# Performance work log

Measured on AMD Instinct MI355X. Metric: run time of the kernel, lower is better.

Reference implementation:

```python
import jax, jax.numpy as jnp
import numpy as np

N, T, D, H, Da = 128, 256, 1024, 1024, 14


def setup_inputs() -> dict:
    key = jax.random.key(0)
    ks = jax.random.split(key, 6)
    x = jax.random.normal(ks[0], (N, T, D), dtype=jnp.float32)
    A = jax.random.normal(ks[1], (N, H, Da, Da), dtype=jnp.float32)
    Wx = jax.random.normal(ks[2], (D, 4 * H), dtype=jnp.float32) / np.sqrt(D)
    Wh = jax.random.normal(ks[3], (H, 4 * H), dtype=jnp.float32) / np.sqrt(H)
    Wattn = jax.random.normal(ks[4], (H, 4 * H), dtype=jnp.float32) / np.sqrt(H)
    b = jnp.zeros((4 * H,), dtype=jnp.float32)
    return {"x": x, "A": A, "Wx": Wx, "Wh": Wh, "Wattn": Wattn, "b": b}


def reference(x, A, Wx, Wh, Wattn, b):
    n, t, d = x.shape
    h_dim = A.shape[1]
    da = A.shape[2]
    scale = 1.0 / np.sqrt(h_dim).astype(np.float32)
    A_flat = A.reshape(n, h_dim, da * da)            # (N, H, P)
    h0 = jnp.mean(A_flat, axis=-1)                   # global avg pool == mean over (2,3)
    c0 = h0

    def step(carry, xt):
        h, c = carry
        # scaled dot-product attention over spatial positions
        scores = jnp.einsum('nh,nhp->np', h, A_flat) * scale   # (N, P)
        w = jax.nn.softmax(scores, axis=-1)
        attn = jnp.einsum('nhp,np->nh', A_flat, w)             # (N, H)
        # fused LSTM gates
        a = xt @ Wx + h @ Wh + attn @ Wattn + b                # (N, 4H)
        ai, af, ao, ag = jnp.split(a, 4, axis=1)
        i = jax.nn.sigmoid(ai)
        f = jax.nn.sigmoid(af)
        o = jax.nn.sigmoid(ao)
        g = jnp.tanh(ag)
        c_next = f * c + i * g
        h_next = o * jnp.tanh(c_next)
        return (h_next, c_next), h_next

    xs = jnp.swapaxes(x, 0, 1)                       # (T, N, D)
    _, hs = jax.lax.scan(step, (h0, c0), xs)         # hs: (T, N, H)
    return jnp.swapaxes(hs, 0, 1)                    # (N, T, H)
```

## Files before the change

kernel.cpp:

```cpp
#include <hip/hip_runtime.h>
#include <math.h>

typedef _Float16 f16;
typedef f16 f16x4 __attribute__((ext_vector_type(4)));
typedef f16 f16x8 __attribute__((ext_vector_type(8)));
typedef float f32x4 __attribute__((ext_vector_type(4)));

#define NB 128
#define TT 256
#define DD 1024
#define HH 1024
#define PP 196
#define K3 3072
#define FOURH 4096
#define NBLK 256
#define NTHR 512
#define WROW 3078
#define LDS_BYTES (16 * WROW * 2 + 9216 * 4)
#define BAR_U32 (8192 + 128 * 64)

__global__ void k_h0(const float* __restrict__ A, float* __restrict__ c0,
                     f16* __restrict__ act_h0) {
  int idx = blockIdx.x * 256 + threadIdx.x;
  const float4* ap = (const float4*)(A + (size_t)idx * PP);
  float s = 0.f;
#pragma unroll
  for (int i = 0; i < PP / 4; ++i) { float4 v = ap[i]; s += v.x + v.y + v.z + v.w; }
  float m = s * (1.0f / PP);
  c0[idx] = m;
  act_h0[idx] = (f16)m;
}

__global__ void k_At(const float* __restrict__ A, f16* __restrict__ A2) {
  __shared__ float tile[32][33];
  int p0 = blockIdx.x * 32, h0 = blockIdx.y * 32, n = blockIdx.z;
  for (int i = threadIdx.x; i < 1024; i += 256) {
    int r = i >> 5, c = i & 31;
    int p = p0 + c;
    float v = 0.f;
    if (p < PP) v = A[((size_t)n * HH + h0 + r) * PP + p];
    tile[r][c] = v;
  }
  __syncthreads();
  for (int i = threadIdx.x; i < 1024; i += 256) {
    int r = i >> 5, c = i & 31;
    int p = p0 + r;
    if (p < PP) A2[((size_t)n * PP + p) * HH + h0 + c] = (f16)tile[c][r];
  }
}

__global__ void k_Wt(const float* __restrict__ Wx, const float* __restrict__ Wh,
                     const float* __restrict__ Wa, f16* __restrict__ Wt) {
  __shared__ float tile[32][33];
  int k0 = blockIdx.x * 32, j0 = blockIdx.y * 32;
  const float* src; int kb;
  if (k0 < 1024)      { src = Wx; kb = k0; }
  else if (k0 < 2048) { src = Wh; kb = k0 - 1024; }
  else                { src = Wa; kb = k0 - 2048; }
  for (int i = threadIdx.x; i < 1024; i += 256) {
    int r = i >> 5, c = i & 31;
    tile[r][c] = src[(size_t)(kb + r) * FOURH + j0 + c];
  }
  __syncthreads();
  for (int i = threadIdx.x; i < 1024; i += 256) {
    int r = i >> 5, c = i & 31;
    Wt[(size_t)(j0 + r) * K3 + k0 + c] = (f16)tile[c][r];
  }
}

__global__ void k_xcvt(const float* __restrict__ x, f16* __restrict__ xh) {
  size_t i = (size_t)blockIdx.x * 256 + threadIdx.x;
  float4 v = ((const float4*)x)[i];
  f16x4 o; o[0] = (f16)v.x; o[1] = (f16)v.y; o[2] = (f16)v.z; o[3] = (f16)v.w;
  *(f16x4*)(xh + i * 4) = o;
}

__device__ __forceinline__ void bar_arrive(unsigned* base, int bx) {
  asm volatile("s_waitcnt vmcnt(0)" ::: "memory");
  unsigned lv = __hip_atomic_fetch_add(base + (bx & 15) * 64, 1u,
                                       __ATOMIC_RELAXED, __HIP_MEMORY_SCOPE_AGENT);
  if ((lv & 15u) == 15u) {
    unsigned rv = __hip_atomic_fetch_add(base + 1024, 1u,
                                         __ATOMIC_RELAXED, __HIP_MEMORY_SCOPE_AGENT);
    if ((rv & 15u) == 15u) {
      unsigned g = (rv >> 4) + 1u;
#pragma unroll
      for (int i = 0; i < 16; ++i)
        __hip_atomic_store(base + 1088 + i * 64, g,
                           __ATOMIC_RELAXED, __HIP_MEMORY_SCOPE_AGENT);
    }
  }
}
__device__ __forceinline__ void bar_wait_acq(unsigned* base, int bx, unsigned target) {
  unsigned* line = base + 1088 + (bx & 15) * 64;
  while (__hip_atomic_load(line, __ATOMIC_RELAXED,
                           __HIP_MEMORY_SCOPE_AGENT) < target)
    __builtin_amdgcn_s_sleep(2);
  (void)__hip_atomic_load(line, __ATOMIC_ACQUIRE, __HIP_MEMORY_SCOPE_AGENT);
}

__device__ __forceinline__ void coh_store_f16(f16* p, f16 v) {
  __hip_atomic_store((short*)p, __builtin_bit_cast(short, v),
                     __ATOMIC_RELAXED, __HIP_MEMORY_SCOPE_AGENT);
}
__device__ __forceinline__ void coh_store_f32(float* p, float v) {
  __hip_atomic_store(p, v, __ATOMIC_RELAXED, __HIP_MEMORY_SCOPE_AGENT);
}
__device__ __forceinline__ float coh_load_f32(const float* p) {
  return __hip_atomic_load(p, __ATOMIC_RELAXED, __HIP_MEMORY_SCOPE_AGENT);
}

__global__ __launch_bounds__(NTHR, 2) void k_steps(
    const f16* __restrict__ xh, const f16* __restrict__ A2,
    const f16* __restrict__ Wtg, const float* __restrict__ bias,
    const float* __restrict__ c0,
    f16* __restrict__ acth0, f16* __restrict__ acth1,
    f16* __restrict__ attnb, float* __restrict__ spart,
    float* __restrict__ out, unsigned* __restrict__ bar) {
  extern __shared__ char smem[];
  f16* wslab = (f16*)smem;
  float* uni   = (float*)(smem + 16 * WROW * 2);
  float* sc    = uni;
  float* wexp  = uni + 208;
  float* srinv = uni + 416;
  float* red   = uni + 512;
  float* slabq = uni;

  int tid = threadIdx.x;
  int lane = tid & 63, wid = tid >> 6;
  int bx = blockIdx.x;
  unsigned* barA = bar;
  unsigned* barG = bar + 4096;
  unsigned* pflag = bar + 8192 + (bx >> 1) * 64;

  int n = bx >> 1, hhalf = bx & 1;
  int hsub = lane & 31;
  int pg = wid * 2 + (lane >> 5);

  f16x8 areg0[13], areg1[13];
  {
    const f16* Ab = A2 + ((size_t)n * PP) * HH + hhalf * 512 + hsub * 16;
#pragma unroll
    for (int i = 0; i < 13; ++i) {
      int p = pg + 16 * i; if (p >= PP) p = pg;
      areg0[i] = *(const f16x8*)(Ab + (size_t)p * HH);
      areg1[i] = *(const f16x8*)(Ab + (size_t)p * HH + 8);
    }
  }

#pragma unroll 1
  for (int c = 0; c < 16; ++c) {
    if (tid < 384) {
      int j = (c >> 2) * 1024 + bx * 4 + (c & 3);
      f16x8 v = *(const f16x8*)(Wtg + (size_t)j * K3 + tid * 8);
      *(f16x8*)(wslab + c * WROW + tid * 8) = v;
    }
  }

  int l15 = lane & 15, quad = lane >> 4;
  int mhalf = wid & 1, kq = wid >> 1;
  int rowbase = mhalf * 64 + l15;
  const f16* wlp = wslab + l15 * WROW + quad * 8;
  int gn = tid >> 2, gh = tid & 3;
  int hs4 = bx * 4;
  float creg = c0[gn * HH + hs4 + gh];
  float b_i = bias[hs4 + gh], b_f = bias[1024 + hs4 + gh];
  float b_o = bias[2048 + hs4 + gh], b_g = bias[3072 + hs4 + gh];

  for (int t = 0; t < TT; ++t) {
    const f16* hcur = (t & 1) ? acth1 : acth0;
    f16* hnxt = (t & 1) ? acth0 : acth1;
    unsigned tgt = (unsigned)(t + 1);

    {
      const f16x8* hp = (const f16x8*)(hcur + (size_t)n * HH + hhalf * 512 + hsub * 16);
      f16x8 hv0 = hp[0], hv1 = hp[1];
      float hf[16];
#pragma unroll
      for (int e = 0; e < 8; ++e) { hf[e] = (float)hv0[e]; hf[8 + e] = (float)hv1[e]; }
#pragma unroll
      for (int i = 0; i < 13; ++i) {
        float s = 0.f;
#pragma unroll
        for (int e = 0; e < 8; ++e)
          s += hf[e] * (float)areg0[i][e] + hf[8 + e] * (float)areg1[i][e];
        s += __shfl_xor(s, 1, 64);
        s += __shfl_xor(s, 2, 64);
        s += __shfl_xor(s, 4, 64);
        s += __shfl_xor(s, 8, 64);
        s += __shfl_xor(s, 16, 64);
        int p = pg + 16 * i;
        if (hsub == 0 && p < PP) {
          sc[p] = s;
          coh_store_f32(spart + bx * 256 + p, s);
        }
      }
    }
    __syncthreads();
    if (tid == 0)
      __hip_atomic_fetch_add(pflag, 1u, __ATOMIC_RELAXED, __HIP_MEMORY_SCOPE_AGENT);

    f32x4 acc4[4];
#pragma unroll
    for (int i = 0; i < 4; ++i)
#pragma unroll
      for (int e = 0; e < 4; ++e) acc4[i][e] = 0.f;

    auto seg = [&](const f16* base, size_t rstride, int kgbase, int nks) {
#pragma unroll 4
      for (int ks = 0; ks < nks; ++ks) {
        const f16* ap = base + ks * 32 + quad * 8;
        f16x8 b = *(const f16x8*)(wlp + kgbase + ks * 32);
        f16x8 a0 = *(const f16x8*)(ap + (size_t)(rowbase)      * rstride);
        f16x8 a1 = *(const f16x8*)(ap + (size_t)(rowbase + 16) * rstride);
        f16x8 a2 = *(const f16x8*)(ap + (size_t)(rowbase + 32) * rstride);
        f16x8 a3 = *(const f16x8*)(ap + (size_t)(rowbase + 48) * rstride);
        acc4[0] = __builtin_amdgcn_mfma_f32_16x16x32_f16(a0, b, acc4[0], 0, 0, 0);
        acc4[1] = __builtin_amdgcn_mfma_f32_16x16x32_f16(a1, b, acc4[1], 0, 0, 0);
        acc4[2] = __builtin_amdgcn_mfma_f32_16x16x32_f16(a2, b, acc4[2], 0, 0, 0);
        acc4[3] = __builtin_amdgcn_mfma_f32_16x16x32_f16(a3, b, acc4[3], 0, 0, 0);
      }
    };
    {
      const f16* xrow = xh + (size_t)t * DD;
      if (kq == 0)      seg(xrow,        (size_t)TT * DD, 0,    16);
      else if (kq == 1) seg(xrow + 512,  (size_t)TT * DD, 512,  16);
      else if (kq == 2) seg(hcur,        HH,              1024, 16);
      else              seg(hcur + 512,  HH,              1536, 16);
    }

    if (tid == 0) {
      while (__hip_atomic_load(pflag, __ATOMIC_RELAXED, __HIP_MEMORY_SCOPE_AGENT)
             < 2u * tgt)
        __builtin_amdgcn_s_sleep(2);
    }
    __syncthreads();
    {
      if (wid == 0) {
        const float* pp = spart + (bx ^ 1) * 256;
        float s0 = (sc[lane]       + coh_load_f32(pp + lane))       * 0.03125f;
        float s1 = (sc[64 + lane]  + coh_load_f32(pp + 64 + lane))  * 0.03125f;
        float s2 = (sc[128 + lane] + coh_load_f32(pp + 128 + lane)) * 0.03125f;
        float s3 = (lane < 4) ? (sc[192 + lane] + coh_load_f32(pp + 192 + lane)) * 0.03125f
                              : -1e30f;
        float mx = fmaxf(fmaxf(s0, s1), fmaxf(s2, s3));
#pragma unroll
        for (int off = 32; off > 0; off >>= 1) mx = fmaxf(mx, __shfl_xor(mx, off, 64));
        float e0 = __expf(s0 - mx), e1 = __expf(s1 - mx), e2 = __expf(s2 - mx);
        float e3 = (lane < 4) ? __expf(s3 - mx) : 0.f;
        float ssum = e0 + e1 + e2 + e3;
#pragma unroll
        for (int off = 32; off > 0; off >>= 1) ssum += __shfl_xor(ssum, off, 64);
        wexp[lane] = e0; wexp[64 + lane] = e1; wexp[128 + lane] = e2;
        if (lane < 4)  wexp[192 + lane] = e3;
        if (lane < 12) wexp[196 + lane] = 0.f;
        if (lane == 0) *srinv = 1.f / ssum;
      }
      __syncthreads();
      float acc[16];
#pragma unroll
      for (int e = 0; e < 16; ++e) acc[e] = 0.f;
#pragma unroll
      for (int i = 0; i < 13; ++i) {
        float wgt = wexp[pg + 16 * i];
#pragma unroll
        for (int e = 0; e < 8; ++e) {
          acc[e]     += wgt * (float)areg0[i][e];
          acc[8 + e] += wgt * (float)areg1[i][e];
        }
      }
#pragma unroll
      for (int e = 0; e < 16; ++e) red[pg * 544 + hsub * 17 + e] = acc[e];
      __syncthreads();
      float s = 0.f;
      int ra = (tid >> 4) * 17 + (tid & 15);
#pragma unroll
      for (int g = 0; g < 16; ++g) s += red[g * 544 + ra];
      coh_store_f16(attnb + (size_t)n * HH + hhalf * 512 + tid,
                    (f16)(s * (*srinv)));
    }
    __syncthreads();
    if (tid == 0) { bar_arrive(barA, bx); bar_wait_acq(barA, bx, tgt); }
    __syncthreads();

    seg(attnb + kq * 256, HH, 2048 + kq * 256, 8);

#pragma unroll
    for (int mt = 0; mt < 4; ++mt)
#pragma unroll
      for (int jr = 0; jr < 4; ++jr)
        slabq[kq * 2304 + (mhalf * 64 + mt * 16 + quad * 4 + jr) * 18 + l15] =
            acc4[mt][jr];
    __syncthreads();
    {
      float ai = b_i, af = b_f, ao = b_o, ag = b_g;
#pragma unroll
      for (int q = 0; q < 4; ++q) {
        const float* sl = slabq + q * 2304 + gn * 18;
        ai += sl[gh]; af += sl[4 + gh]; ao += sl[8 + gh]; ag += sl[12 + gh];
      }
      float ig = 1.f / (1.f + __expf(-ai));
      float fg = 1.f / (1.f + __expf(-af));
      float og = 1.f / (1.f + __expf(-ao));
      float gg = tanhf(ag);
      creg = fg * creg + ig * gg;
      float hn = og * tanhf(creg);
      __builtin_nontemporal_store(hn, &out[((size_t)gn * TT + t) * HH + hs4 + gh]);
      coh_store_f16(hnxt + gn * HH + hs4 + gh, (f16)hn);
    }
    __syncthreads();
    if (tid == 0) { bar_arrive(barG, bx); bar_wait_acq(barG, bx, tgt); }
    __syncthreads();
  }
}

extern "C" void kernel_launch(void* const* d_in, const int* in_sizes, int n_in,
                              void* d_out, int out_size, void* d_ws, size_t ws_size,
                              hipStream_t stream) {
  const float* x  = (const float*)d_in[0];
  const float* A  = (const float*)d_in[1];
  const float* Wx = (const float*)d_in[2];
  const float* Wh = (const float*)d_in[3];
  const float* Wa = (const float*)d_in[4];
  const float* b  = (const float*)d_in[5];
  float* out = (float*)d_out;

  char* ws = (char*)d_ws;
  f16* A2 = (f16*)ws;          ws += (size_t)NB * PP * HH * 2;
  f16* Wt = (f16*)ws;          ws += (size_t)FOURH * K3 * 2;
  f16* xh = (f16*)ws;          ws += (size_t)NB * TT * DD * 2;
  f16* acth0 = (f16*)ws;       ws += (size_t)NB * HH * 2;
  f16* acth1 = (f16*)ws;       ws += (size_t)NB * HH * 2;
  f16* attnb = (f16*)ws;       ws += (size_t)NB * HH * 2;
  float* c0 = (float*)ws;      ws += (size_t)NB * HH * 4;
  float* spart = (float*)ws;   ws += (size_t)NBLK * 256 * 4;
  unsigned* bar = (unsigned*)ws; ws += (size_t)BAR_U32 * 4;

  static int attr_set = 0;
  if (!attr_set) {
    hipFuncSetAttribute((const void*)k_steps,
                        hipFuncAttributeMaxDynamicSharedMemorySize, LDS_BYTES);
    attr_set = 1;
  }

  hipMemsetAsync(bar, 0, BAR_U32 * 4, stream);
  k_h0<<<512, 256, 0, stream>>>(A, c0, acth0);
  k_At<<<dim3(7, 32, NB), 256, 0, stream>>>(A, A2);
  k_Wt<<<dim3(96, 128), 256, 0, stream>>>(Wx, Wh, Wa, Wt);
  k_xcvt<<<32768, 256, 0, stream>>>(x, xh);

  void* args[] = { (void*)&xh, (void*)&A2, (void*)&Wt, (void*)&b, (void*)&c0,
                   (void*)&acth0, (void*)&acth1, (void*)&attnb, (void*)&spart,
                   (void*)&out, (void*)&bar };
  hipLaunchCooperativeKernel((const void*)k_steps, dim3(NBLK), dim3(NTHR),
                             args, LDS_BYTES, stream);
}
```

Baseline: 12.71 ms.

## Overlap next-step x projection with grid barrier and use fdot2 for scores

The input-projection MFMA work for step t+1 (x @ Wx) now runs between arriving at and waiting on the global barrier, so it hides behind barrier latency instead of sitting on the critical path. The K split is rebalanced so each wave group does 8 k-steps of x, 8 of h and 8 of attn, rather than some groups taking 16 x-steps and others 16 h-steps. The attention score dot products switch to packed f16 fdot2 instructions, and the spin-wait sleep is shortened. Risks include fdot2 changing accumulation precision and more polling traffic on the atomics.

Measured after the change: 15.01 ms. +18.1%, slower.

```diff
diff --git a/kernel.cpp b/kernel.cpp
--- a/kernel.cpp
+++ b/kernel.cpp
@@ -2,6 +2,7 @@
 #include <math.h>
 
 typedef _Float16 f16;
+typedef f16 f16x2 __attribute__((ext_vector_type(2)));
 typedef f16 f16x4 __attribute__((ext_vector_type(4)));
 typedef f16 f16x8 __attribute__((ext_vector_type(8)));
 typedef float f32x4 __attribute__((ext_vector_type(4)));
@@ -19,6 +20,13 @@
 #define LDS_BYTES (16 * WROW * 2 + 9216 * 4)
 #define BAR_U32 (8192 + 128 * 64)
 
+#if __has_builtin(__builtin_amdgcn_fdot2)
+#define FDOT2(a, b, c) __builtin_amdgcn_fdot2((a), (b), (c), false)
+#else
+#define FDOT2(a, b, c) \
+  ((c) + (float)(a)[0] * (float)(b)[0] + (float)(a)[1] * (float)(b)[1])
+#endif
+
 __global__ void k_h0(const float* __restrict__ A, float* __restrict__ c0,
                      f16* __restrict__ act_h0) {
   int idx = blockIdx.x * 256 + threadIdx.x;
@@ -95,7 +103,7 @@
   unsigned* line = base + 1088 + (bx & 15) * 64;
   while (__hip_atomic_load(line, __ATOMIC_RELAXED,
                            __HIP_MEMORY_SCOPE_AGENT) < target)
-    __builtin_amdgcn_s_sleep(2);
+    __builtin_amdgcn_s_sleep(1);
   (void)__hip_atomic_load(line, __ATOMIC_ACQUIRE, __HIP_MEMORY_SCOPE_AGENT);
 }
 
@@ -167,6 +175,32 @@
   float b_i = bias[hs4 + gh], b_f = bias[1024 + hs4 + gh];
   float b_o = bias[2048 + hs4 + gh], b_g = bias[3072 + hs4 + gh];
 
+  f32x4 acc4[4];
+#pragma unroll
+  for (int i = 0; i < 4; ++i)
+#pragma unroll
+    for (int e = 0; e < 4; ++e) acc4[i][e] = 0.f;
+
+  auto seg = [&](const f16* base, size_t rstride, int kgbase, int nks) {
+#pragma unroll 4
+    for (int ks = 0; ks < nks; ++ks) {
+      const f16* ap = base + ks * 32 + quad * 8;
+      f16x8 b = *(const f16x8*)(wlp + kgbase + ks * 32);
+      f16x8 a0 = *(const f16x8*)(ap + (size_t)(rowbase)      * rstride);
+      f16x8 a1 = *(const f16x8*)(ap + (size_t)(rowbase + 16) * rstride);
+      f16x8 a2 = *(const f16x8*)(ap + (size_t)(rowbase + 32) * rstride);
+      f16x8 a3 = *(const f16x8*)(ap + (size_t)(rowbase + 48) * rstride);
+      acc4[0] = __builtin_amdgcn_mfma_f32_16x16x32_f16(a0, b, acc4[0], 0, 0, 0);
+      acc4[1] = __builtin_amdgcn_mfma_f32_16x16x32_f16(a1, b, acc4[1], 0, 0, 0);
+      acc4[2] = __builtin_amdgcn_mfma_f32_16x16x32_f16(a2, b, acc4[2], 0, 0, 0);
+      acc4[3] = __builtin_amdgcn_mfma_f32_16x16x32_f16(a3, b, acc4[3], 0, 0, 0);
+    }
+  };
+
+  __syncthreads();
+
+  seg(xh + kq * 256, (size_t)TT * DD, kq * 256, 8);
+
   for (int t = 0; t < TT; ++t) {
     const f16* hcur = (t & 1) ? acth1 : acth0;
     f16* hnxt = (t & 1) ? acth0 : acth1;
@@ -175,15 +209,20 @@
     {
       const f16x8* hp = (const f16x8*)(hcur + (size_t)n * HH + hhalf * 512 + hsub * 16);
       f16x8 hv0 = hp[0], hv1 = hp[1];
-      float hf[16];
-#pragma unroll
-      for (int e = 0; e < 8; ++e) { hf[e] = (float)hv0[e]; hf[8 + e] = (float)hv1[e]; }
+      f16x2 h2[8];
+#pragma unroll
+      for (int j = 0; j < 4; ++j) {
+        h2[j]     = *(((const f16x2*)&hv0) + j);
+        h2[4 + j] = *(((const f16x2*)&hv1) + j);
+      }
 #pragma unroll
       for (int i = 0; i < 13; ++i) {
         float s = 0.f;
 #pragma unroll
-        for (int e = 0; e < 8; ++e)
-          s += hf[e] * (float)areg0[i][e] + hf[8 + e] * (float)areg1[i][e];
+        for (int j = 0; j < 4; ++j) {
+          s = FDOT2(*(((const f16x2*)&areg0[i]) + j), h2[j], s);
+          s = FDOT2(*(((const f16x2*)&areg1[i]) + j), h2[4 + j], s);
+        }
         s += __shfl_xor(s, 1, 64);
         s += __shfl_xor(s, 2, 64);
         s += __shfl_xor(s, 4, 64);
@@ -200,39 +239,12 @@
     if (tid == 0)
       __hip_atomic_fetch_add(pflag, 1u, __ATOMIC_RELAXED, __HIP_MEMORY_SCOPE_AGENT);
 
-    f32x4 acc4[4];
-#pragma unroll
-    for (int i = 0; i < 4; ++i)
-#pragma unroll
-      for (int e = 0; e < 4; ++e) acc4[i][e] = 0.f;
-
-    auto seg = [&](const f16* base, size_t rstride, int kgbase, int nks) {
-#pragma unroll 4
-      for (int ks = 0; ks < nks; ++ks) {
-        const f16* ap = base + ks * 32 + quad * 8;
-        f16x8 b = *(const f16x8*)(wlp + kgbase + ks * 32);
-        f16x8 a0 = *(const f16x8*)(ap + (size_t)(rowbase)      * rstride);
-        f16x8 a1 = *(const f16x8*)(ap + (size_t)(rowbase + 16) * rstride);
-        f16x8 a2 = *(const f16x8*)(ap + (size_t)(rowbase + 32) * rstride);
-        f16x8 a3 = *(const f16x8*)(ap + (size_t)(rowbase + 48) * rstride);
-        acc4[0] = __builtin_amdgcn_mfma_f32_16x16x32_f16(a0, b, acc4[0], 0, 0, 0);
-        acc4[1] = __builtin_amdgcn_mfma_f32_16x16x32_f16(a1, b, acc4[1], 0, 0, 0);
-        acc4[2] = __builtin_amdgcn_mfma_f32_16x16x32_f16(a2, b, acc4[2], 0, 0, 0);
-        acc4[3] = __builtin_amdgcn_mfma_f32_16x16x32_f16(a3, b, acc4[3], 0, 0, 0);
-      }
-    };
-    {
-      const f16* xrow = xh + (size_t)t * DD;
-      if (kq == 0)      seg(xrow,        (size_t)TT * DD, 0,    16);
-      else if (kq == 1) seg(xrow + 512,  (size_t)TT * DD, 512,  16);
-      else if (kq == 2) seg(hcur,        HH,              1024, 16);
-      else              seg(hcur + 512,  HH,              1536, 16);
-    }
+    seg(hcur + kq * 256, HH, 1024 + kq * 256, 8);
 
     if (tid == 0) {
       while (__hip_atomic_load(pflag, __ATOMIC_RELAXED, __HIP_MEMORY_SCOPE_AGENT)
              < 2u * tgt)
-        __builtin_amdgcn_s_sleep(2);
+        __builtin_amdgcn_s_sleep(1);
     }
     __syncthreads();
     {
@@ -291,6 +303,10 @@
       for (int jr = 0; jr < 4; ++jr)
         slabq[kq * 2304 + (mhalf * 64 + mt * 16 + quad * 4 + jr) * 18 + l15] =
             acc4[mt][jr];
+#pragma unroll
+    for (int i = 0; i < 4; ++i)
+#pragma unroll
+      for (int e = 0; e < 4; ++e) acc4[i][e] = 0.f;
     __syncthreads();
     {
       float ai = b_i, af = b_f, ao = b_o, ag = b_g;
@@ -309,8 +325,13 @@
       coh_store_f16(hnxt + gn * HH + hs4 + gh, (f16)hn);
     }
     __syncthreads();
-    if (tid == 0) { bar_arrive(barG, bx); bar_wait_acq(barG, bx, tgt); }
-    __syncthreads();
+
+    if (t + 1 < TT) {
+      if (tid == 0) bar_arrive(barG, bx);
+      seg(xh + (size_t)(t + 1) * DD + kq * 256, (size_t)TT * DD, kq * 256, 8);
+      if (tid == 0) bar_wait_acq(barG, bx, tgt);
+      __syncthreads();
+    }
   }
 }
 
```
